# Performance work log

Hardware: AMD Instinct MI355X
Metric: run time of the kernel (lower is better)

Reference implementation:

```python
import jax, jax.numpy as jnp
import numpy as np

B, S, D, H = 2, 2048, 1024, 16
HD = D // H  # head dim 64

def setup_inputs() -> dict:
    key = jax.random.key(0)
    k1, k2, k3 = jax.random.split(key, 3)
    x = jax.random.normal(k1, (B, S, D), dtype=jnp.float32)
    w_attn = jax.random.normal(k2, (D, 3 * D), dtype=jnp.float32) * (1.0 / np.sqrt(D))
    w_proj = jax.random.normal(k3, (D, D), dtype=jnp.float32) * (1.0 / np.sqrt(D))
    return {"x": x, "w_attn": w_attn, "w_proj": w_proj}

def reference(x, w_attn, w_proj):
    b, s, d = x.shape
    qkv = x @ w_attn                      # [b, s, 3d]
    q, k, v = jnp.split(qkv, 3, axis=-1)
    def heads(t):
        return t.reshape(b, s, H, HD).transpose(0, 2, 1, 3)  # [b, h, s, hd]
    q, k, v = heads(q), heads(k), heads(v)
    scale = 1.0 / np.sqrt(HD)
    att = jnp.einsum('bhqd,bhkd->bhqk', q, k) * scale        # [b, h, s, s]
    causal = jnp.tril(jnp.ones((s, s), dtype=bool))
    att = jnp.where(causal[None, None], att, -jnp.inf)
    att = jax.nn.softmax(att, axis=-1)
    y = jnp.einsum('bhqk,bhkd->bhqd', att, v)                # [b, h, s, hd]
    y = y.transpose(0, 2, 1, 3).reshape(b, s, d)
    return y @ w_proj
```

## Files before the change

kernel.cpp:

```cpp
#include <hip/hip_runtime.h>

#define B_  2
#define S_  2048
#define D_  1024
#define H_  16
#define HD_ 64
#define TD_ 3072

typedef __bf16 bf16x8 __attribute__((ext_vector_type(8)));
typedef float  f32x4  __attribute__((ext_vector_type(4)));
typedef float  f32x16 __attribute__((ext_vector_type(16)));

#define AS1 __attribute__((address_space(1)))
#define AS3 __attribute__((address_space(3)))

#define MASKVAL (-60000.0f)
#define MINITVAL (-30000.0f)

__device__ __forceinline__ unsigned short f2bf(float f) {
  return __builtin_bit_cast(unsigned short, (__bf16)f);
}

__device__ __forceinline__ unsigned int pkbf(float lo, float hi) {
  unsigned int r;
  asm("v_cvt_pk_bf16_f32 %0, %1, %2" : "=v"(r) : "v"(lo), "v"(hi));
  return r;
}

__device__ __forceinline__ void plswap(unsigned int& a, unsigned int& b) {
  asm volatile("v_permlane32_swap_b32 %0, %1" : "+v"(a), "+v"(b));
}

__device__ __forceinline__ float exp2a(float x) {
  return __builtin_amdgcn_exp2f(x);
}

__device__ __forceinline__ float xmax32(float x) {
  return fmaxf(x, __shfl_xor(x, 32, 64));
}
__device__ __forceinline__ float xadd32(float x) {
  return x + __shfl_xor(x, 32, 64);
}

__device__ __forceinline__ void gload16(const void* g, void* l) {
  __builtin_amdgcn_global_load_lds((const AS1 void*)g, (AS3 void*)l, 16, 0, 0);
}

__global__ __launch_bounds__(256) void k_convert_x(const float* __restrict__ x,
                                                   unsigned short* __restrict__ xb) {
  const int i = (blockIdx.x * 256 + threadIdx.x) * 4;
  float4 v = *(const float4*)(x + i);
  ushort4 o;
  o.x = f2bf(v.x); o.y = f2bf(v.y); o.z = f2bf(v.z); o.w = f2bf(v.w);
  *(ushort4*)(xb + i) = o;
}

__global__ __launch_bounds__(256) void k_transpose_w(const float* __restrict__ w,
                                                     unsigned short* __restrict__ wt,
                                                     int R, int C) {
  __shared__ __align__(16) unsigned short tile[64][72];
  const int t = threadIdx.x;
  const int c0 = blockIdx.x * 64, r0 = blockIdx.y * 64;
  const int rr = t >> 2, cc = (t & 3) * 16;
  const float* src = w + (size_t)(r0 + rr) * C + c0 + cc;
#pragma unroll
  for (int j = 0; j < 16; j += 4) {
    float4 v = *(const float4*)(src + j);
    tile[rr][cc + j + 0] = f2bf(v.x);
    tile[rr][cc + j + 1] = f2bf(v.y);
    tile[rr][cc + j + 2] = f2bf(v.z);
    tile[rr][cc + j + 3] = f2bf(v.w);
  }
  __syncthreads();
  unsigned short* dst = wt + (size_t)(c0 + rr) * R + r0 + cc;
#pragma unroll
  for (int j = 0; j < 16; j += 2) {
    unsigned int pk = (unsigned int)tile[cc + j][rr] |
                      ((unsigned int)tile[cc + j + 1][rr] << 16);
    *(unsigned int*)(dst + j) = pk;
  }
}

__global__ __launch_bounds__(256) void k_pack_kv(const unsigned short* __restrict__ qkv,
                                                 unsigned short* __restrict__ kp,
                                                 unsigned short* __restrict__ vp) {
  __shared__ __align__(16) unsigned short vl[64][72];
  const int t = threadIdx.x;
  const int bx = blockIdx.x;
  const int bh = blockIdx.y;
  const int b = bh >> 4, h = bh & 15;
  if (bx < 64) {
    const int tau = bx;
    const int c = t >> 6, hi = (t >> 5) & 1, l = t & 31;
    const unsigned short* src =
        qkv + (size_t)(b * S_ + 32 * tau + l) * TD_ + D_ + h * HD_ + c * 16 + hi * 8;
    uint4 v = *(const uint4*)src;
    *(uint4*)(kp + (size_t)bh * 131072 + tau * 2048 + t * 8) = v;
  } else {
    const int tau2 = bx - 64;
#pragma unroll
    for (int it = 0; it < 2; ++it) {
      const int idx = it * 256 + t;
      const int row = idx >> 3, cq = (idx & 7) * 8;
      *(uint4*)&vl[row][cq] =
          *(const uint4*)(qkv + (size_t)(b * S_ + 64 * tau2 + row) * TD_ +
                          2 * D_ + h * HD_ + cq);
    }
    __syncthreads();
#pragma unroll
    for (int it = 0; it < 2; ++it) {
      const int tid = it * 256 + t;
      const int T = (tid >> 8) & 1, c = (tid >> 7) & 1;
      const int half = (tid >> 6) & 1, hi = (tid >> 5) & 1, l = tid & 31;
      const int srow = T * 32 + c * 16 + hi * 8;
      const int hd = half * 32 + l;
      unsigned int wv[4];
#pragma unroll
      for (int jj = 0; jj < 4; ++jj)
        wv[jj] = (unsigned int)vl[srow + 2 * jj][hd] |
                 ((unsigned int)vl[srow + 2 * jj + 1][hd] << 16);
      uint4 o; o.x = wv[0]; o.y = wv[1]; o.z = wv[2]; o.w = wv[3];
      *(uint4*)(vp + (size_t)bh * 131072 + tau2 * 4096 + tid * 8) = o;
    }
  }
}

template <int BF16_OUT>
__global__ __launch_bounds__(256) void k_gemm_bt(const unsigned short* __restrict__ A,
                                                 const unsigned short* __restrict__ Bt,
                                                 void* __restrict__ Cv,
                                                 int Ndim, int K) {
  __shared__ __align__(16) unsigned short ldsA[128 * 64];
  __shared__ __align__(16) unsigned short ldsB[128 * 64];
  const int t = threadIdx.x;
  const int lane = t & 63;
  const int wid = t >> 6;
  const int wr = wid >> 1, wc = wid & 1;
  const int bx = blockIdx.x;
  const int bm = blockIdx.y * 128;
  const int bn = (((bx & 7) * 3) + (bx >> 3)) * 128;
  const int r = lane & 15, g = lane >> 4;

  f32x4 acc[4][4] = {};

  for (int kt = 0; kt < K; kt += 64) {
#pragma unroll
    for (int c = 0; c < 4; ++c) {
      const int idx = c * 256 + t;
      const int row = idx >> 3;
      const int col = ((idx & 7) ^ (row & 7)) * 8;
      gload16(A + (size_t)(bm + row) * K + kt + col, ldsA + idx * 8);
      gload16(Bt + (size_t)(bn + row) * K + kt + col, ldsB + idx * 8);
    }
    asm volatile("s_waitcnt vmcnt(0)" ::: "memory");
    __syncthreads();
#pragma unroll
    for (int ks = 0; ks < 2; ++ks) {
      bf16x8 af[4], bfr[4];
#pragma unroll
      for (int m = 0; m < 4; ++m) {
        const int row = wr * 64 + m * 16 + r;
        const int slot = (ks * 4 + g) ^ (row & 7);
        af[m] = *(const bf16x8*)(ldsA + row * 64 + slot * 8);
      }
#pragma unroll
      for (int n = 0; n < 4; ++n) {
        const int row = wc * 64 + n * 16 + r;
        const int slot = (ks * 4 + g) ^ (row & 7);
        bfr[n] = *(const bf16x8*)(ldsB + row * 64 + slot * 8);
      }
#pragma unroll
      for (int m = 0; m < 4; ++m)
#pragma unroll
        for (int n = 0; n < 4; ++n)
          acc[m][n] = __builtin_amdgcn_mfma_f32_16x16x32_bf16(af[m], bfr[n],
                                                              acc[m][n], 0, 0, 0);
    }
    __syncthreads();
  }

  const int row0 = bm + wr * 64 + g * 4;
  const int col0 = bn + wc * 64 + r;
  if constexpr (BF16_OUT) {
    unsigned short* C = (unsigned short*)Cv;
#pragma unroll
    for (int m = 0; m < 4; ++m)
#pragma unroll
      for (int n = 0; n < 4; ++n)
#pragma unroll
        for (int i = 0; i < 4; ++i)
          C[(size_t)(row0 + m * 16 + i) * Ndim + col0 + n * 16] = f2bf(acc[m][n][i]);
  } else {
    float* C = (float*)Cv;
#pragma unroll
    for (int m = 0; m < 4; ++m)
#pragma unroll
      for (int n = 0; n < 4; ++n)
#pragma unroll
        for (int i = 0; i < 4; ++i)
          C[(size_t)(row0 + m * 16 + i) * Ndim + col0 + n * 16] = acc[m][n][i];
  }
}

__global__ __launch_bounds__(256) void k_gemm_bt64(const unsigned short* __restrict__ A,
                                                   const unsigned short* __restrict__ Bt,
                                                   float* __restrict__ C,
                                                   int Ndim, int K) {
  __shared__ __align__(16) unsigned short ldsA[64 * 64];
  __shared__ __align__(16) unsigned short ldsB[128 * 64];
  const int t = threadIdx.x;
  const int lane = t & 63;
  const int wid = t >> 6;
  const int wr = wid >> 1, wc = wid & 1;
  const int bm = blockIdx.y * 64, bn = blockIdx.x * 128;
  const int r = lane & 15, g = lane >> 4;

  f32x4 acc[2][4] = {};

  for (int kt = 0; kt < K; kt += 64) {
#pragma unroll
    for (int c = 0; c < 2; ++c) {
      const int idx = c * 256 + t;
      const int row = idx >> 3;
      const int col = ((idx & 7) ^ (row & 7)) * 8;
      gload16(A + (size_t)(bm + row) * K + kt + col, ldsA + idx * 8);
    }
#pragma unroll
    for (int c = 0; c < 4; ++c) {
      const int idx = c * 256 + t;
      const int row = idx >> 3;
      const int col = ((idx & 7) ^ (row & 7)) * 8;
      gload16(Bt + (size_t)(bn + row) * K + kt + col, ldsB + idx * 8);
    }
    asm volatile("s_waitcnt vmcnt(0)" ::: "memory");
    __syncthreads();
#pragma unroll
    for (int ks = 0; ks < 2; ++ks) {
      bf16x8 af[2], bfr[4];
#pragma unroll
      for (int m = 0; m < 2; ++m) {
        const int row = wr * 32 + m * 16 + r;
        const int slot = (ks * 4 + g) ^ (row & 7);
        af[m] = *(const bf16x8*)(ldsA + row * 64 + slot * 8);
      }
#pragma unroll
      for (int n = 0; n < 4; ++n) {
        const int row = wc * 64 + n * 16 + r;
        const int slot = (ks * 4 + g) ^ (row & 7);
        bfr[n] = *(const bf16x8*)(ldsB + row * 64 + slot * 8);
      }
#pragma unroll
      for (int m = 0; m < 2; ++m)
#pragma unroll
        for (int n = 0; n < 4; ++n)
          acc[m][n] = __builtin_amdgcn_mfma_f32_16x16x32_bf16(af[m], bfr[n],
                                                              acc[m][n], 0, 0, 0);
    }
    __syncthreads();
  }

  const int row0 = bm + wr * 32 + g * 4;
  const int col0 = bn + wc * 64 + r;
#pragma unroll
  for (int m = 0; m < 2; ++m)
#pragma unroll
    for (int n = 0; n < 4; ++n)
#pragma unroll
      for (int i = 0; i < 4; ++i)
        C[(size_t)(row0 + m * 16 + i) * Ndim + col0 + n * 16] = acc[m][n][i];
}

__global__ __launch_bounds__(256, 4) void k_attn(const unsigned short* __restrict__ qkv,
                                                 const unsigned short* __restrict__ kp,
                                                 const unsigned short* __restrict__ vp,
                                                 unsigned short* __restrict__ y) {
  __shared__ __align__(16) float Om[2][64][32];
  __shared__ float Ml[2][2][32];
  const int t = threadIdx.x;
  const int lane = t & 63, w = t >> 6;
  const int l31 = lane & 31, hi = lane >> 5;
  const int pr = w & 1;
  const int parity = w >> 1;
  const int bh = blockIdx.x & 31;
  const int j = blockIdx.x >> 5;
  const int sj = pr ? (63 - j) : j;
  const int h = bh & 15, b = bh >> 4;
  const int qbase = 32 * sj;
  const int qq = qbase + l31;

  const float SC = 0.125f * 1.44269504f;

  bf16x8 qf[4];
  {
    const unsigned short* qp = qkv + (size_t)(b * S_ + qbase + l31) * TD_ + h * HD_;
#pragma unroll
    for (int c = 0; c < 4; ++c) {
      bf16x8 rl = *(const bf16x8*)(qp + c * 16 + hi * 8);
      union { unsigned int u[4]; bf16x8 v; } pl;
#pragma unroll
      for (int jx = 0; jx < 4; ++jx)
        pl.u[jx] = pkbf((float)rl[2 * jx] * SC, (float)rl[2 * jx + 1] * SC);
      qf[c] = pl.v;
    }
  }

  float mr = MINITVAL, lr = 0.f;
  f32x16 o0 = {}, o1 = {};

  const unsigned short* kpb = kp + (size_t)bh * 131072;
  const unsigned short* vpb = vp + (size_t)bh * 131072;

  const int tmax = (32 * sj + 31) >> 6;

  for (int kvt = parity; kvt <= tmax; kvt += 2) {
    const int kv0 = kvt << 6;
    bf16x8 kf[2][4];
#pragma unroll
    for (int T = 0; T < 2; ++T)
#pragma unroll
      for (int c = 0; c < 4; ++c)
        kf[T][c] = *(const bf16x8*)(kpb + (size_t)(kvt * 8 + T * 4 + c) * 512 +
                                    lane * 8);

    f32x16 s0 = {}, s1 = {};
    __builtin_amdgcn_s_setprio(1);
#pragma unroll
    for (int c = 0; c < 4; ++c) {
      s0 = __builtin_amdgcn_mfma_f32_32x32x16_bf16(kf[0][c], qf[c], s0, 0, 0, 0);
      s1 = __builtin_amdgcn_mfma_f32_32x32x16_bf16(kf[1][c], qf[c], s1, 0, 0, 0);
    }
    __builtin_amdgcn_s_setprio(0);

    float am[4] = {MASKVAL, MASKVAL, MASKVAL, MASKVAL};
    if (kv0 + 63 > qbase) {
#pragma unroll
      for (int rg = 0; rg < 16; ++rg) {
        const int kv = kv0 + (rg & 3) + 8 * (rg >> 2) + 4 * hi;
        float v0 = (kv <= qq) ? s0[rg] : MASKVAL; s0[rg] = v0;
        float v1 = (kv + 32 <= qq) ? s1[rg] : MASKVAL; s1[rg] = v1;
        am[rg & 3] = fmaxf(am[rg & 3], fmaxf(v0, v1));
      }
    } else {
#pragma unroll
      for (int rg = 0; rg < 16; ++rg)
        am[rg & 3] = fmaxf(am[rg & 3], fmaxf(s0[rg], s1[rg]));
    }
    const float pm = xmax32(fmaxf(fmaxf(am[0], am[1]), fmaxf(am[2], am[3])));

    const float nm = fmaxf(mr, pm);
    if (!__all(nm - mr <= 12.0f)) {
      const float cr = exp2a(mr - nm);
      mr = nm;
      lr *= cr;
#pragma unroll
      for (int rg = 0; rg < 16; ++rg) { o0[rg] *= cr; o1[rg] *= cr; }
    }

    float as[4] = {0.f, 0.f, 0.f, 0.f};
#pragma unroll
    for (int rg = 0; rg < 16; ++rg) {
      const float p0 = exp2a(s0[rg] - mr); s0[rg] = p0;
      const float p1 = exp2a(s1[rg] - mr); s1[rg] = p1;
      as[rg & 3] += p0 + p1;
    }
    lr += xadd32((as[0] + as[1]) + (as[2] + as[3]));

    const unsigned short* vpt = vpb + (size_t)kvt * 4096;
    __builtin_amdgcn_s_setprio(1);
#pragma unroll
    for (int T = 0; T < 2; ++T) {
      const f32x16& sT = T ? s1 : s0;
#pragma unroll
      for (int c = 0; c < 2; ++c) {
        unsigned int x0 = pkbf(sT[8 * c + 0], sT[8 * c + 1]);
        unsigned int x1 = pkbf(sT[8 * c + 2], sT[8 * c + 3]);
        unsigned int x2 = pkbf(sT[8 * c + 4], sT[8 * c + 5]);
        unsigned int x3 = pkbf(sT[8 * c + 6], sT[8 * c + 7]);
        plswap(x0, x2);
        plswap(x1, x3);
        union { unsigned int u[4]; bf16x8 v; } pb;
        pb.u[0] = x0; pb.u[1] = x1; pb.u[2] = x2; pb.u[3] = x3;
        const unsigned short* vb = vpt + (size_t)((T * 2 + c) * 2) * 512 + lane * 8;
        bf16x8 vf0 = *(const bf16x8*)(vb);
        bf16x8 vf1 = *(const bf16x8*)(vb + 512);
        o0 = __builtin_amdgcn_mfma_f32_32x32x16_bf16(vf0, pb.v, o0, 0, 0, 0);
        o1 = __builtin_amdgcn_mfma_f32_32x32x16_bf16(vf1, pb.v, o1, 0, 0, 0);
      }
    }
    __builtin_amdgcn_s_setprio(0);
  }

  __syncthreads();
  if (parity) {
#pragma unroll
    for (int tt = 0; tt < 2; ++tt) {
      const f32x16& o = tt ? o1 : o0;
#pragma unroll
      for (int rg = 0; rg < 16; ++rg) {
        const int row = tt * 32 + (rg & 3) + 8 * (rg >> 2) + 4 * hi;
        Om[pr][row][l31] = o[rg];
      }
    }
    if (!hi) {
      Ml[pr][0][l31] = mr;
      Ml[pr][1][l31] = lr;
    }
  }
  __syncthreads();
  if (!parity) {
    const float mo = Ml[pr][0][l31];
    const float lo2 = Ml[pr][1][l31];
    const float mm = fmaxf(mr, mo);
    const float ce = exp2a(mr - mm), co = exp2a(mo - mm);
    const float lt = lr * ce + lo2 * co;
    const float ic = ce / lt, io = co / lt;
    unsigned short* yp = y + (size_t)(b * S_ + qbase + l31) * D_ + h * HD_;
#pragma unroll
    for (int tt = 0; tt < 2; ++tt) {
      const f32x16& o = tt ? o1 : o0;
#pragma unroll
      for (int rg = 0; rg < 16; rg += 2) {
        const int row = tt * 32 + (rg & 3) + 8 * (rg >> 2) + 4 * hi;
        const float v0 = o[rg] * ic + Om[pr][row][l31] * io;
        const float v1 = o[rg + 1] * ic + Om[pr][row + 1][l31] * io;
        *(unsigned int*)(yp + row) = pkbf(v0, v1);
      }
    }
  }
}

extern "C" void kernel_launch(void* const* d_in, const int* in_sizes, int n_in,
                              void* d_out, int out_size, void* d_ws, size_t ws_size,
                              hipStream_t stream) {
  const float* x  = (const float*)d_in[0];
  const float* wa = (const float*)d_in[1];
  const float* wp = (const float*)d_in[2];
  float* out = (float*)d_out;

  char* ws = (char*)d_ws;
  unsigned short* xb  = (unsigned short*)(ws + 0);
  unsigned short* kp  = (unsigned short*)(ws + 0);
  unsigned short* waT = (unsigned short*)(ws + 8388608);
  unsigned short* wpT = (unsigned short*)(ws + 14680064);
  unsigned short* qkv = (unsigned short*)(ws + 16777216);
  unsigned short* vp  = (unsigned short*)(ws + 41943040);
  unsigned short* yb  = (unsigned short*)(ws + 50331648);

  k_convert_x<<<4096, 256, 0, stream>>>(x, xb);
  k_transpose_w<<<dim3(48, 16), 256, 0, stream>>>(wa, waT, D_, TD_);
  k_transpose_w<<<dim3(16, 16), 256, 0, stream>>>(wp, wpT, D_, D_);
  k_gemm_bt<1><<<dim3(24, 32), 256, 0, stream>>>(xb, waT, qkv, TD_, D_);
  k_pack_kv<<<dim3(96, 32), 256, 0, stream>>>(qkv, kp, vp);
  k_attn<<<1024, 256, 0, stream>>>(qkv, kp, vp, yb);
  k_gemm_bt64<<<dim3(8, 64), 256, 0, stream>>>(yb, wpT, out, D_, D_);
}
```

Baseline: 115.1 us.

## Fuse K/V packing into QKV GEMM epilogue and merge weight transposes

The QKV GEMM epilogue now writes Q row-major and scatters K and V directly into the packed per-head layouts the attention kernel expects, which removes the separate pack kernel and its read-back of the qkv buffer. The two weight-transpose launches are also merged into one kernel with a combined grid. The cost is a more scattered epilogue store pattern (2-byte and 8-byte strided writes) in the GEMM, and a reshuffled workspace layout.

```diff
diff --git a/kernel.cpp b/kernel.cpp
--- a/kernel.cpp
+++ b/kernel.cpp
@@ -55,12 +55,20 @@
   *(ushort4*)(xb + i) = o;
 }
 
-__global__ __launch_bounds__(256) void k_transpose_w(const float* __restrict__ w,
-                                                     unsigned short* __restrict__ wt,
-                                                     int R, int C) {
+__global__ __launch_bounds__(256) void k_prep_w(const float* __restrict__ wa,
+                                                const float* __restrict__ wp,
+                                                unsigned short* __restrict__ waT,
+                                                unsigned short* __restrict__ wpT) {
   __shared__ __align__(16) unsigned short tile[64][72];
   const int t = threadIdx.x;
-  const int c0 = blockIdx.x * 64, r0 = blockIdx.y * 64;
+  const int bx = blockIdx.x;
+  const float* w;
+  unsigned short* wt;
+  int C, c0;
+  if (bx < 48) { w = wa; wt = waT; C = TD_; c0 = bx * 64; }
+  else         { w = wp; wt = wpT; C = D_;  c0 = (bx - 48) * 64; }
+  const int R = D_;
+  const int r0 = blockIdx.y * 64;
   const int rr = t >> 2, cc = (t & 3) * 16;
   const float* src = w + (size_t)(r0 + rr) * C + c0 + cc;
 #pragma unroll
@@ -81,57 +89,14 @@
   }
 }
 
-__global__ __launch_bounds__(256) void k_pack_kv(const unsigned short* __restrict__ qkv,
-                                                 unsigned short* __restrict__ kp,
-                                                 unsigned short* __restrict__ vp) {
-  __shared__ __align__(16) unsigned short vl[64][72];
-  const int t = threadIdx.x;
-  const int bx = blockIdx.x;
-  const int bh = blockIdx.y;
-  const int b = bh >> 4, h = bh & 15;
-  if (bx < 64) {
-    const int tau = bx;
-    const int c = t >> 6, hi = (t >> 5) & 1, l = t & 31;
-    const unsigned short* src =
-        qkv + (size_t)(b * S_ + 32 * tau + l) * TD_ + D_ + h * HD_ + c * 16 + hi * 8;
-    uint4 v = *(const uint4*)src;
-    *(uint4*)(kp + (size_t)bh * 131072 + tau * 2048 + t * 8) = v;
-  } else {
-    const int tau2 = bx - 64;
-#pragma unroll
-    for (int it = 0; it < 2; ++it) {
-      const int idx = it * 256 + t;
-      const int row = idx >> 3, cq = (idx & 7) * 8;
-      *(uint4*)&vl[row][cq] =
-          *(const uint4*)(qkv + (size_t)(b * S_ + 64 * tau2 + row) * TD_ +
-                          2 * D_ + h * HD_ + cq);
-    }
-    __syncthreads();
-#pragma unroll
-    for (int it = 0; it < 2; ++it) {
-      const int tid = it * 256 + t;
-      const int T = (tid >> 8) & 1, c = (tid >> 7) & 1;
-      const int half = (tid >> 6) & 1, hi = (tid >> 5) & 1, l = tid & 31;
-      const int srow = T * 32 + c * 16 + hi * 8;
-      const int hd = half * 32 + l;
-      unsigned int wv[4];
-#pragma unroll
-      for (int jj = 0; jj < 4; ++jj)
-        wv[jj] = (unsigned int)vl[srow + 2 * jj][hd] |
-                 ((unsigned int)vl[srow + 2 * jj + 1][hd] << 16);
-      uint4 o; o.x = wv[0]; o.y = wv[1]; o.z = wv[2]; o.w = wv[3];
-      *(uint4*)(vp + (size_t)bh * 131072 + tau2 * 4096 + tid * 8) = o;
-    }
-  }
-}
-
-template <int BF16_OUT>
-__global__ __launch_bounds__(256) void k_gemm_bt(const unsigned short* __restrict__ A,
-                                                 const unsigned short* __restrict__ Bt,
-                                                 void* __restrict__ Cv,
-                                                 int Ndim, int K) {
+__global__ __launch_bounds__(256) void k_gemm_qkv(const unsigned short* __restrict__ A,
+                                                  const unsigned short* __restrict__ Bt,
+                                                  unsigned short* __restrict__ qb,
+                                                  unsigned short* __restrict__ kp,
+                                                  unsigned short* __restrict__ vp) {
   __shared__ __align__(16) unsigned short ldsA[128 * 64];
   __shared__ __align__(16) unsigned short ldsB[128 * 64];
+  const int K = D_;
   const int t = threadIdx.x;
   const int lane = t & 63;
   const int wid = t >> 6;
@@ -181,24 +146,55 @@
 
   const int row0 = bm + wr * 64 + g * 4;
   const int col0 = bn + wc * 64 + r;
-  if constexpr (BF16_OUT) {
-    unsigned short* C = (unsigned short*)Cv;
+  const int region = bn >> 10;
+  const int b = blockIdx.y >> 4;
+  const int sbase = (bm & 2047) + wr * 64 + g * 4;
+
+  if (region == 0) {
 #pragma unroll
     for (int m = 0; m < 4; ++m)
 #pragma unroll
       for (int n = 0; n < 4; ++n)
 #pragma unroll
         for (int i = 0; i < 4; ++i)
-          C[(size_t)(row0 + m * 16 + i) * Ndim + col0 + n * 16] = f2bf(acc[m][n][i]);
+          qb[(size_t)(row0 + m * 16 + i) * D_ + col0 + n * 16] = f2bf(acc[m][n][i]);
+  } else if (region == 1) {
+    const int h = ((bn - 1024) >> 6) + wc;
+    unsigned short* kpb = kp + (size_t)(b * 16 + h) * 131072;
+#pragma unroll
+    for (int m = 0; m < 4; ++m) {
+      const int s = sbase + m * 16;
+      const int tau = s >> 5, l = s & 31;
+#pragma unroll
+      for (int n = 0; n < 4; ++n) {
+        unsigned short* kq = kpb + tau * 2048 +
+                             (n * 64 + (r >> 3) * 32 + l) * 8 + (r & 7);
+        kq[0]  = f2bf(acc[m][n][0]);
+        kq[8]  = f2bf(acc[m][n][1]);
+        kq[16] = f2bf(acc[m][n][2]);
+        kq[24] = f2bf(acc[m][n][3]);
+      }
+    }
   } else {
-    float* C = (float*)Cv;
-#pragma unroll
-    for (int m = 0; m < 4; ++m)
-#pragma unroll
-      for (int n = 0; n < 4; ++n)
-#pragma unroll
-        for (int i = 0; i < 4; ++i)
-          C[(size_t)(row0 + m * 16 + i) * Ndim + col0 + n * 16] = acc[m][n][i];
+    const int h = ((bn - 2048) >> 6) + wc;
+    unsigned short* vpb = vp + (size_t)(b * 16 + h) * 131072;
+#pragma unroll
+    for (int m = 0; m < 4; ++m) {
+      const int s = sbase + m * 16;
+      const int tau2 = s >> 6;
+      const int T = (s >> 5) & 1, c16 = (s >> 4) & 1, hi8 = (s >> 3) & 1;
+      const int u = s & 7;
+#pragma unroll
+      for (int n = 0; n < 4; ++n) {
+        const int half = n >> 1;
+        const int l = (n & 1) * 16 + r;
+        const int tid = T * 256 + c16 * 128 + half * 64 + hi8 * 32 + l;
+        unsigned long long pk2 =
+            (unsigned long long)pkbf(acc[m][n][0], acc[m][n][1]) |
+            ((unsigned long long)pkbf(acc[m][n][2], acc[m][n][3]) << 32);
+        *(unsigned long long*)(vpb + tau2 * 4096 + tid * 8 + u) = pk2;
+      }
+    }
   }
 }
 
@@ -270,7 +266,7 @@
         C[(size_t)(row0 + m * 16 + i) * Ndim + col0 + n * 16] = acc[m][n][i];
 }
 
-__global__ __launch_bounds__(256, 4) void k_attn(const unsigned short* __restrict__ qkv,
+__global__ __launch_bounds__(256, 4) void k_attn(const unsigned short* __restrict__ qb,
                                                  const unsigned short* __restrict__ kp,
                                                  const unsigned short* __restrict__ vp,
                                                  unsigned short* __restrict__ y) {
@@ -292,7 +288,7 @@
 
   bf16x8 qf[4];
   {
-    const unsigned short* qp = qkv + (size_t)(b * S_ + qbase + l31) * TD_ + h * HD_;
+    const unsigned short* qp = qb + (size_t)(b * S_ + qbase + l31) * D_ + h * HD_;
 #pragma unroll
     for (int c = 0; c < 4; ++c) {
       bf16x8 rl = *(const bf16x8*)(qp + c * 16 + hi * 8);
@@ -439,18 +435,16 @@
 
   char* ws = (char*)d_ws;
   unsigned short* xb  = (unsigned short*)(ws + 0);
-  unsigned short* kp  = (unsigned short*)(ws + 0);
   unsigned short* waT = (unsigned short*)(ws + 8388608);
   unsigned short* wpT = (unsigned short*)(ws + 14680064);
-  unsigned short* qkv = (unsigned short*)(ws + 16777216);
-  unsigned short* vp  = (unsigned short*)(ws + 41943040);
-  unsigned short* yb  = (unsigned short*)(ws + 50331648);
+  unsigned short* qb  = (unsigned short*)(ws + 16777216);
+  unsigned short* kp  = (unsigned short*)(ws + 25165824);
+  unsigned short* vp  = (unsigned short*)(ws + 33554432);
+  unsigned short* yb  = (unsigned short*)(ws + 41943040);
 
   k_convert_x<<<4096, 256, 0, stream>>>(x, xb);
-  k_transpose_w<<<dim3(48, 16), 256, 0, stream>>>(wa, waT, D_, TD_);
-  k_transpose_w<<<dim3(16, 16), 256, 0, stream>>>(wp, wpT, D_, D_);
-  k_gemm_bt<1><<<dim3(24, 32), 256, 0, stream>>>(xb, waT, qkv, TD_, D_);
-  k_pack_kv<<<dim3(96, 32), 256, 0, stream>>>(qkv, kp, vp);
-  k_attn<<<1024, 256, 0, stream>>>(qkv, kp, vp, yb);
+  k_prep_w<<<dim3(64, 16), 256, 0, stream>>>(wa, wp, waT, wpT);
+  k_gemm_qkv<<<dim3(24, 32), 256, 0, stream>>>(xb, waT, qb, kp, vp);
+  k_attn<<<1024, 256, 0, stream>>>(qb, kp, vp, yb);
   k_gemm_bt64<<<dim3(8, 64), 256, 0, stream>>>(yb, wpT, out, D_, D_);
 }
```

Result: no change. 115.3 us (+0.1%).
